# Kernel tuning notes

Measured on AMD Instinct MI355X. Metric: run time of the kernel, lower is better.

## Reference

```python
import jax, jax.numpy as jnp
import numpy as np

EPS = 1e-12  # torch F.normalize eps


def setup_inputs() -> dict:
    key = jax.random.key(0)
    k1, k2, k3 = jax.random.split(key, 3)
    B, D, H, W, K = 64, 512, 32, 32, 64
    x = jax.random.normal(k1, (B, D, H, W), dtype=jnp.float32)
    w = jax.random.normal(k2, (K, D), dtype=jnp.float32) * 0.05  # 1x1 conv weight
    c = jax.random.normal(k3, (K, D), dtype=jnp.float32)          # cluster centers
    return {"x": x, "w": w, "c": c}


def reference(x, w, c):
    B, D, H, W = x.shape
    K = w.shape[0]
    N = H * W
    # 1x1 conv (no bias): (B,D,H,W) x (K,D) -> (B,K,H,W)
    features = jnp.einsum('bdhw,kd->bkhw', x, w)
    # NOTE: original applies softmax over dim=2 (the H axis only)
    a_bar = jax.nn.softmax(features, axis=2)
    xf = x.reshape(B, D, N)
    a = a_bar.reshape(B, K, N)
    # V[b,k,d] = sum_n a[b,k,n] * (x[b,d,n] - c[k,d])
    V = jnp.einsum('bkn,bdn->bkd', a, xf) - a.sum(axis=2)[:, :, None] * c[None]
    V = V.transpose(2, 1, 0)  # (D, K, B)
    # F.normalize(V, p=2, dim=1) applied twice (second is idempotent)
    norm = jnp.maximum(jnp.linalg.norm(V, axis=1, keepdims=True), EPS)
    y = V / norm
    norm2 = jnp.maximum(jnp.linalg.norm(y, axis=1, keepdims=True), EPS)
    return y / norm2
```

## Files before the change

kernel.cpp:

```cpp
#include <hip/hip_runtime.h>


typedef __attribute__((ext_vector_type(8))) short short8;
typedef __attribute__((ext_vector_type(4))) float f32x4;
typedef unsigned short u16;
typedef unsigned int u32;

union S8u { u32 q[4]; short8 s; };

__device__ __forceinline__ u32 pk2(float lo, float hi) {
  union { float f; u32 u; } a, b; a.f = lo; b.f = hi;
  u32 xl = (a.u + 0x7fffu + ((a.u >> 16) & 1u)) >> 16;
  u32 xh = (b.u + 0x7fffu + ((b.u >> 16) & 1u)) & 0xffff0000u;
  return xl | xh;
}

__device__ __forceinline__ u16 bf1(float f) {
  union { float f; u32 u; } a; a.f = f;
  return (u16)((a.u + 0x7fffu + ((a.u >> 16) & 1u)) >> 16);
}

typedef const __attribute__((address_space(1))) u32 GU32;
typedef __attribute__((address_space(3))) u32 LU32;
__device__ __forceinline__ void glds16(const void* g, void* l) {
  __builtin_amdgcn_global_load_lds((GU32*)g, (LU32*)l, 16, 0, 0);
}

__global__ __launch_bounds__(256) void k0_packw(
    const float* __restrict__ w, u16* __restrict__ wsw)
{
  const int tg = blockIdx.x * 256 + threadIdx.x;
  const int dd4 = tg & 7, i = (tg >> 3) & 15, k = tg >> 7;
  f32x4 v = *(const f32x4*)(w + k * 512 + i * 32 + dd4 * 4);
  u32* dst = (u32*)(wsw + ((size_t)i * 64 + k) * 40 + dd4 * 4);
  dst[0] = pk2(v[0], v[1]);
  dst[1] = pk2(v[2], v[3]);
}

__global__ __launch_bounds__(256, 2) void k1_features(
    const float* __restrict__ x, const u16* __restrict__ wsw,
    float* __restrict__ feat)
{
  const int blk = blockIdx.x;
  const int b = blk & 63, nt8 = blk >> 6;
  const int nb = nt8 * 128;
  const int tid = threadIdx.x, lane = tid & 63, wv = tid >> 6;
  const int row = lane & 15, q = lane >> 4;

  __shared__ __align__(16) float xs[2][32][128];
  __shared__ __align__(16) u16 wls[2][64][40];

  const char* xbase = (const char*)(x + ((size_t)b << 19) + nb);
  const char* wbase = (const char*)wsw;
  const int dd0 = tid >> 5, cby = (tid & 31) * 16;

  f32x4 acc[4][2];
#pragma unroll
  for (int mt = 0; mt < 4; mt++)
#pragma unroll
    for (int nt = 0; nt < 2; nt++) acc[mt][nt] = (f32x4){0.f, 0.f, 0.f, 0.f};

#define STAGE1(d0, buf)                                                        \
  {                                                                            \
    char* lx = (char*)&xs[buf][0][0];                                          \
    _Pragma("unroll")                                                          \
    for (int j = 0; j < 4; j++) {                                              \
      const int dd = j * 8 + dd0;                                              \
      glds16(xbase + (size_t)((d0) + dd) * 4096 + cby,                         \
             lx + j * 4096 + tid * 16);                                        \
    }                                                                          \
    char* lw = (char*)&wls[buf][0][0];                                         \
    const char* gw = wbase + (size_t)((d0) >> 5) * 5120;                       \
    glds16(gw + tid * 16, lw + tid * 16);                                      \
    if (tid < 64) glds16(gw + 4096 + tid * 16, lw + 4096 + tid * 16);          \
  }

  STAGE1(0, 0);
  for (int i = 0; i < 16; i++) {
    const int buf = i & 1;
    __syncthreads();
    if (i < 15) STAGE1((i + 1) * 32, buf ^ 1);

    short8 af[4];
#pragma unroll
    for (int mt = 0; mt < 4; mt++)
      af[mt] = *(const short8*)&wls[buf][mt * 16 + row][q * 8];
    short8 bfv[2];
#pragma unroll
    for (int nt = 0; nt < 2; nt++) {
      const int n = wv * 32 + nt * 16 + row;
      const int d8 = q * 8;
      float v0 = xs[buf][d8 + 0][n], v1 = xs[buf][d8 + 1][n];
      float v2 = xs[buf][d8 + 2][n], v3 = xs[buf][d8 + 3][n];
      float v4 = xs[buf][d8 + 4][n], v5 = xs[buf][d8 + 5][n];
      float v6 = xs[buf][d8 + 6][n], v7 = xs[buf][d8 + 7][n];
      S8u t;
      t.q[0] = pk2(v0, v1); t.q[1] = pk2(v2, v3);
      t.q[2] = pk2(v4, v5); t.q[3] = pk2(v6, v7);
      bfv[nt] = t.s;
    }
#pragma unroll
    for (int nt = 0; nt < 2; nt++)
#pragma unroll
      for (int mt = 0; mt < 4; mt++)
        acc[mt][nt] = __builtin_amdgcn_mfma_f32_16x16x32_bf16(af[mt], bfv[nt], acc[mt][nt], 0, 0, 0);
  }
#undef STAGE1

  float* fb = feat + ((size_t)b << 16);
  const int nbw = nb + wv * 32;
#pragma unroll
  for (int mt = 0; mt < 4; mt++)
#pragma unroll
    for (int nt = 0; nt < 2; nt++)
#pragma unroll
      for (int r = 0; r < 4; r++)
        fb[(mt * 16 + q * 4 + r) * 1024 + nbw + nt * 16 + row] = acc[mt][nt][r];
}

__global__ __launch_bounds__(256) void k1b_softmax(
    const float* __restrict__ feat, u16* __restrict__ apad)
{
  const int tid = threadIdx.x, lane = tid & 63, wv = tid >> 6;
  const int rid = blockIdx.x * 4 + wv;
  const int b = rid >> 6, k = rid & 63;
  const float* f = feat + ((size_t)rid << 10);
  const int w = lane & 31, half = lane >> 5;
  const int base = w + half * 512;
  float v[16];
  float m = -1e30f;
#pragma unroll
  for (int i = 0; i < 16; i++) { v[i] = f[base + i * 32]; m = fmaxf(m, v[i]); }
  m = fmaxf(m, __shfl_xor(m, 32));
  float s = 0.f;
#pragma unroll
  for (int i = 0; i < 16; i++) { v[i] = __expf(v[i] - m); s += v[i]; }
  s += __shfl_xor(s, 32);
  const float inv = 1.0f / s;
#pragma unroll
  for (int i = 0; i < 16; i++) {
    const int h = half * 16 + i;
    apad[((size_t)(b * 32 + h) * 64 + k) * 40 + w] = bf1(v[i] * inv);
  }
}

__global__ __launch_bounds__(256, 2) void k2_aggregate(
    const float* __restrict__ x, const u16* __restrict__ apad,
    const float* __restrict__ cc, float* __restrict__ yw)
{
  const int blk = blockIdx.x;
  const int b = blk & 63, dt = blk >> 6;
  const int tid = threadIdx.x, lane = tid & 63, wv = tid >> 6;
  const int row = lane & 15, q = lane >> 4;

  __shared__ __align__(16) u16 als[2][64][40];

  const char* abase = (const char*)(apad + (size_t)b * 32 * 64 * 40);
  const float* px0 = x + ((size_t)b << 19) + (size_t)(dt * 64 + wv * 16 + row) * 1024 + q * 8;

#define STAGEA(i, buf)                                                         \
  {                                                                            \
    char* la = (char*)&als[buf][0][0];                                         \
    const char* ga = abase + (size_t)(i) * 5120;                               \
    glds16(ga + tid * 16, la + tid * 16);                                      \
    if (tid < 64) glds16(ga + 4096 + tid * 16, la + 4096 + tid * 16);          \
  }

  f32x4 acc[4];
#pragma unroll
  for (int mt = 0; mt < 4; mt++) acc[mt] = (f32x4){0.f, 0.f, 0.f, 0.f};

  STAGEA(0, 0);
  f32x4 c0 = *(const f32x4*)px0;
  f32x4 c1 = *(const f32x4*)(px0 + 4);
  f32x4 p0, p1;
  for (int i = 0; i < 32; i++) {
    const int buf = i & 1;
    __syncthreads();
    if (i < 31) {
      STAGEA(i + 1, buf ^ 1);
      p0 = *(const f32x4*)(px0 + (i + 1) * 32);
      p1 = *(const f32x4*)(px0 + (i + 1) * 32 + 4);
    }
    S8u t;
    t.q[0] = pk2(c0[0], c0[1]); t.q[1] = pk2(c0[2], c0[3]);
    t.q[2] = pk2(c1[0], c1[1]); t.q[3] = pk2(c1[2], c1[3]);
    const short8 bfv = t.s;
#pragma unroll
    for (int mt = 0; mt < 4; mt++) {
      short8 af = *(const short8*)&als[buf][mt * 16 + row][q * 8];
      acc[mt] = __builtin_amdgcn_mfma_f32_16x16x32_bf16(af, bfv, acc[mt], 0, 0, 0);
    }
    c0 = p0; c1 = p1;
  }
#undef STAGEA

  const int dcol = dt * 64 + wv * 16 + row;
  float v[16]; float ss = 0.f;
#pragma unroll
  for (int mt = 0; mt < 4; mt++)
#pragma unroll
    for (int r = 0; r < 4; r++) {
      const int k = mt * 16 + q * 4 + r;
      const float tv = acc[mt][r] - 32.0f * cc[k * 512 + dcol];
      v[mt * 4 + r] = tv; ss += tv * tv;
    }
  ss += __shfl_xor(ss, 16);
  ss += __shfl_xor(ss, 32);
  const float rn = 1.0f / fmaxf(sqrtf(ss), 1e-12f);
  float* yb = yw + ((size_t)b << 15) + dcol;
#pragma unroll
  for (int mt = 0; mt < 4; mt++)
#pragma unroll
    for (int r = 0; r < 4; r++)
      yb[(size_t)(mt * 16 + q * 4 + r) << 9] = v[mt * 4 + r] * rn;
}

__global__ __launch_bounds__(256) void k3_transpose(
    const float* __restrict__ yw, float* __restrict__ out)
{
  const int blk = blockIdx.x;
  const int k = blk & 63;
  const int dt = blk >> 6;
  const int d0 = dt * 64;
  const int tid = threadIdx.x;
  __shared__ float T[64][68];
  {
    const int bl = tid >> 2, seg = tid & 3;
    const float* src = yw + (size_t)bl * 32768 + k * 512 + d0 + seg * 16;
#pragma unroll
    for (int i = 0; i < 4; i++) {
      f32x4 v = *(const f32x4*)(src + i * 4);
#pragma unroll
      for (int jj = 0; jj < 4; jj++) T[seg * 16 + i * 4 + jj][bl] = v[jj];
    }
  }
  __syncthreads();
  {
    const int dl = tid >> 2, bseg = tid & 3;
    float* dst = out + (size_t)(d0 + dl) * 4096 + k * 64 + bseg * 16;
    const float* srcT = &T[dl][bseg * 16];
#pragma unroll
    for (int i = 0; i < 4; i++)
      *(f32x4*)(dst + i * 4) = *(const f32x4*)(srcT + i * 4);
  }
}

extern "C" void kernel_launch(void* const* d_in, const int* in_sizes, int n_in,
                              void* d_out, int out_size, void* d_ws, size_t ws_size,
                              hipStream_t stream) {
  const float* x = (const float*)d_in[0];
  const float* w = (const float*)d_in[1];
  const float* c = (const float*)d_in[2];
  float* out = (float*)d_out;
  char* ws = (char*)d_ws;
  float* feat = (float*)ws;
  u16*   apad = (u16*)(ws + (size_t)16 * 1024 * 1024);
  float* yw   = (float*)(ws + (size_t)26 * 1024 * 1024);
  u16*   wsw  = (u16*)(ws + (size_t)34 * 1024 * 1024);
  k0_packw    <<<dim3(32),   dim3(256), 0, stream>>>(w, wsw);
  k1_features <<<dim3(512),  dim3(256), 0, stream>>>(x, wsw, feat);
  k1b_softmax <<<dim3(1024), dim3(256), 0, stream>>>(feat, apad);
  k2_aggregate<<<dim3(512),  dim3(256), 0, stream>>>(x, apad, c, yw);
  k3_transpose<<<dim3(512),  dim3(256), 0, stream>>>(yw, out);
}
```

Measured before the change: 231.9 us.

## Drop weight-pack kernel, load weights and softmax output directly into registers

The separate weight-packing kernel is removed. k1 now loads fp32 weights straight from global into registers with a one-step prefetch and converts them to bf16 in-loop, so weights no longer go through LDS. The softmax writes its output in plain row-major bf16 instead of a padded tiled layout. k2 now reads the attention operand directly from global into registers, while x is staged through a swizzled LDS buffer via global_load_lds. This removes one kernel launch and the LDS traffic for weights and attention, at the cost of more global loads per wave and extra conversion ALU work.

```diff
diff --git a/kernel.cpp b/kernel.cpp
--- a/kernel.cpp
+++ b/kernel.cpp
@@ -26,19 +26,8 @@
   __builtin_amdgcn_global_load_lds((GU32*)g, (LU32*)l, 16, 0, 0);
 }
 
-__global__ __launch_bounds__(256) void k0_packw(
-    const float* __restrict__ w, u16* __restrict__ wsw)
-{
-  const int tg = blockIdx.x * 256 + threadIdx.x;
-  const int dd4 = tg & 7, i = (tg >> 3) & 15, k = tg >> 7;
-  f32x4 v = *(const f32x4*)(w + k * 512 + i * 32 + dd4 * 4);
-  u32* dst = (u32*)(wsw + ((size_t)i * 64 + k) * 40 + dd4 * 4);
-  dst[0] = pk2(v[0], v[1]);
-  dst[1] = pk2(v[2], v[3]);
-}
-
 __global__ __launch_bounds__(256, 2) void k1_features(
-    const float* __restrict__ x, const u16* __restrict__ wsw,
+    const float* __restrict__ x, const float* __restrict__ wgt,
     float* __restrict__ feat)
 {
   const int blk = blockIdx.x;
@@ -48,11 +37,10 @@
   const int row = lane & 15, q = lane >> 4;
 
   __shared__ __align__(16) float xs[2][32][128];
-  __shared__ __align__(16) u16 wls[2][64][40];
 
   const char* xbase = (const char*)(x + ((size_t)b << 19) + nb);
-  const char* wbase = (const char*)wsw;
   const int dd0 = tid >> 5, cby = (tid & 31) * 16;
+  const float* wrow = wgt + row * 512 + q * 8;
 
   f32x4 acc[4][2];
 #pragma unroll
@@ -64,27 +52,39 @@
   {                                                                            \
     char* lx = (char*)&xs[buf][0][0];                                          \
     _Pragma("unroll")                                                          \
-    for (int j = 0; j < 4; j++) {                                              \
-      const int dd = j * 8 + dd0;                                              \
-      glds16(xbase + (size_t)((d0) + dd) * 4096 + cby,                         \
+    for (int j = 0; j < 4; j++)                                                \
+      glds16(xbase + (size_t)((d0) + j * 8 + dd0) * 4096 + cby,                \
              lx + j * 4096 + tid * 16);                                        \
-    }                                                                          \
-    char* lw = (char*)&wls[buf][0][0];                                         \
-    const char* gw = wbase + (size_t)((d0) >> 5) * 5120;                       \
-    glds16(gw + tid * 16, lw + tid * 16);                                      \
-    if (tid < 64) glds16(gw + 4096 + tid * 16, lw + 4096 + tid * 16);          \
   }
 
   STAGE1(0, 0);
+  f32x4 wa[4][2];
+#pragma unroll
+  for (int mt = 0; mt < 4; mt++) {
+    wa[mt][0] = *(const f32x4*)(wrow + mt * 8192);
+    wa[mt][1] = *(const f32x4*)(wrow + mt * 8192 + 4);
+  }
+
   for (int i = 0; i < 16; i++) {
     const int buf = i & 1;
     __syncthreads();
-    if (i < 15) STAGE1((i + 1) * 32, buf ^ 1);
-
     short8 af[4];
 #pragma unroll
-    for (int mt = 0; mt < 4; mt++)
-      af[mt] = *(const short8*)&wls[buf][mt * 16 + row][q * 8];
+    for (int mt = 0; mt < 4; mt++) {
+      S8u t;
+      t.q[0] = pk2(wa[mt][0][0], wa[mt][0][1]); t.q[1] = pk2(wa[mt][0][2], wa[mt][0][3]);
+      t.q[2] = pk2(wa[mt][1][0], wa[mt][1][1]); t.q[3] = pk2(wa[mt][1][2], wa[mt][1][3]);
+      af[mt] = t.s;
+    }
+    if (i < 15) {
+      STAGE1((i + 1) * 32, buf ^ 1);
+      const float* wn = wrow + (i + 1) * 32;
+#pragma unroll
+      for (int mt = 0; mt < 4; mt++) {
+        wa[mt][0] = *(const f32x4*)(wn + mt * 8192);
+        wa[mt][1] = *(const f32x4*)(wn + mt * 8192 + 4);
+      }
+    }
     short8 bfv[2];
 #pragma unroll
     for (int nt = 0; nt < 2; nt++) {
@@ -119,12 +119,12 @@
 }
 
 __global__ __launch_bounds__(256) void k1b_softmax(
-    const float* __restrict__ feat, u16* __restrict__ apad)
+    const float* __restrict__ feat, u16* __restrict__ am)
 {
   const int tid = threadIdx.x, lane = tid & 63, wv = tid >> 6;
   const int rid = blockIdx.x * 4 + wv;
-  const int b = rid >> 6, k = rid & 63;
   const float* f = feat + ((size_t)rid << 10);
+  u16* ar = am + ((size_t)rid << 10);
   const int w = lane & 31, half = lane >> 5;
   const int base = w + half * 512;
   float v[16];
@@ -138,14 +138,11 @@
   s += __shfl_xor(s, 32);
   const float inv = 1.0f / s;
 #pragma unroll
-  for (int i = 0; i < 16; i++) {
-    const int h = half * 16 + i;
-    apad[((size_t)(b * 32 + h) * 64 + k) * 40 + w] = bf1(v[i] * inv);
-  }
+  for (int i = 0; i < 16; i++) ar[base + i * 32] = bf1(v[i] * inv);
 }
 
 __global__ __launch_bounds__(256, 2) void k2_aggregate(
-    const float* __restrict__ x, const u16* __restrict__ apad,
+    const float* __restrict__ x, const u16* __restrict__ am,
     const float* __restrict__ cc, float* __restrict__ yw)
 {
   const int blk = blockIdx.x;
@@ -153,47 +150,60 @@
   const int tid = threadIdx.x, lane = tid & 63, wv = tid >> 6;
   const int row = lane & 15, q = lane >> 4;
 
-  __shared__ __align__(16) u16 als[2][64][40];
-
-  const char* abase = (const char*)(apad + (size_t)b * 32 * 64 * 40);
-  const float* px0 = x + ((size_t)b << 19) + (size_t)(dt * 64 + wv * 16 + row) * 1024 + q * 8;
-
-#define STAGEA(i, buf)                                                         \
+  __shared__ __align__(16) float xs[2][2048];
+
+  const char* xbase = (const char*)(x + ((size_t)b << 19) + (size_t)dt * 64 * 1024);
+  const u16* ab = am + ((size_t)b << 16) + row * 1024 + q * 8;
+  const int r0 = tid >> 3, s0g = tid & 7;
+
+#define STAGE2(n0, buf)                                                        \
   {                                                                            \
-    char* la = (char*)&als[buf][0][0];                                         \
-    const char* ga = abase + (size_t)(i) * 5120;                               \
-    glds16(ga + tid * 16, la + tid * 16);                                      \
-    if (tid < 64) glds16(ga + 4096 + tid * 16, la + 4096 + tid * 16);          \
+    char* lxs = (char*)&xs[buf][0];                                            \
+    _Pragma("unroll")                                                          \
+    for (int j = 0; j < 2; j++) {                                              \
+      const int r = j * 32 + r0;                                               \
+      const int col = ((s0g * 4) + ((r & 3) << 3)) & 31;                       \
+      glds16(xbase + (size_t)r * 4096 + (size_t)((n0) + col) * 4,              \
+             lxs + (j * 256 + tid) * 16);                                      \
+    }                                                                          \
   }
 
   f32x4 acc[4];
 #pragma unroll
   for (int mt = 0; mt < 4; mt++) acc[mt] = (f32x4){0.f, 0.f, 0.f, 0.f};
 
-  STAGEA(0, 0);
-  f32x4 c0 = *(const f32x4*)px0;
-  f32x4 c1 = *(const f32x4*)(px0 + 4);
-  f32x4 p0, p1;
+  STAGE2(0, 0);
+  short8 sa[4];
+#pragma unroll
+  for (int mt = 0; mt < 4; mt++) sa[mt] = *(const short8*)(ab + mt * 16384);
+
+  const int rB = wv * 16 + row;
+  const int slot = (2 * q - 2 * (rB & 3)) & 7;
+  const int fidx = rB * 32 + slot * 4;
+
   for (int i = 0; i < 32; i++) {
     const int buf = i & 1;
     __syncthreads();
+    short8 af[4];
+#pragma unroll
+    for (int mt = 0; mt < 4; mt++) af[mt] = sa[mt];
     if (i < 31) {
-      STAGEA(i + 1, buf ^ 1);
-      p0 = *(const f32x4*)(px0 + (i + 1) * 32);
-      p1 = *(const f32x4*)(px0 + (i + 1) * 32 + 4);
-    }
+      STAGE2((i + 1) * 32, buf ^ 1);
+      const u16* an = ab + (i + 1) * 32;
+#pragma unroll
+      for (int mt = 0; mt < 4; mt++) sa[mt] = *(const short8*)(an + mt * 16384);
+    }
+    f32x4 g0 = *(const f32x4*)&xs[buf][fidx];
+    f32x4 g1 = *(const f32x4*)&xs[buf][fidx + 4];
     S8u t;
-    t.q[0] = pk2(c0[0], c0[1]); t.q[1] = pk2(c0[2], c0[3]);
-    t.q[2] = pk2(c1[0], c1[1]); t.q[3] = pk2(c1[2], c1[3]);
+    t.q[0] = pk2(g0[0], g0[1]); t.q[1] = pk2(g0[2], g0[3]);
+    t.q[2] = pk2(g1[0], g1[1]); t.q[3] = pk2(g1[2], g1[3]);
     const short8 bfv = t.s;
 #pragma unroll
-    for (int mt = 0; mt < 4; mt++) {
-      short8 af = *(const short8*)&als[buf][mt * 16 + row][q * 8];
-      acc[mt] = __builtin_amdgcn_mfma_f32_16x16x32_bf16(af, bfv, acc[mt], 0, 0, 0);
-    }
-    c0 = p0; c1 = p1;
-  }
-#undef STAGEA
+    for (int mt = 0; mt < 4; mt++)
+      acc[mt] = __builtin_amdgcn_mfma_f32_16x16x32_bf16(af[mt], bfv, acc[mt], 0, 0, 0);
+  }
+#undef STAGE2
 
   const int dcol = dt * 64 + wv * 16 + row;
   float v[16]; float ss = 0.f;
@@ -255,12 +265,10 @@
   float* out = (float*)d_out;
   char* ws = (char*)d_ws;
   float* feat = (float*)ws;
-  u16*   apad = (u16*)(ws + (size_t)16 * 1024 * 1024);
+  u16*   a_ws = (u16*)(ws + (size_t)17 * 1024 * 1024);
   float* yw   = (float*)(ws + (size_t)26 * 1024 * 1024);
-  u16*   wsw  = (u16*)(ws + (size_t)34 * 1024 * 1024);
-  k0_packw    <<<dim3(32),   dim3(256), 0, stream>>>(w, wsw);
-  k1_features <<<dim3(512),  dim3(256), 0, stream>>>(x, wsw, feat);
-  k1b_softmax <<<dim3(1024), dim3(256), 0, stream>>>(feat, apad);
-  k2_aggregate<<<dim3(512),  dim3(256), 0, stream>>>(x, apad, c, yw);
+  k1_features <<<dim3(512),  dim3(256), 0, stream>>>(x, w, feat);
+  k1b_softmax <<<dim3(1024), dim3(256), 0, stream>>>(feat, a_ws);
+  k2_aggregate<<<dim3(512),  dim3(256), 0, stream>>>(x, a_ws, c, yw);
   k3_transpose<<<dim3(512),  dim3(256), 0, stream>>>(yw, out);
 }
```

Measured after the change: 237.9 us. 2.6% more time.
